# Kernel optimization log

Hardware: AMD Instinct MI355X
Metric: run time of the kernel (lower is better)

The kernel has to match this reference:

```python
import jax, jax.numpy as jnp
import numpy as np


def _conv3x3(x, w, b):
    # standard 3x3 conv, stride 1, padding 1 (NCHW / OIHW)
    y = jax.lax.conv_general_dilated(x, w, window_strides=(1, 1),
                                     padding=((1, 1), (1, 1)),
                                     dimension_numbers=('NCHW', 'OIHW', 'NCHW'))
    return y + b[None, :, None, None]


def _bilinear_gather(img, py, px):
    # img [B,C,H,W]; py/px [B,K,H,W] fractional sample coords; zero outside (torchvision semantics)
    B, C, H, W = img.shape
    K = py.shape[1]
    y0f = jnp.floor(py)
    x0f = jnp.floor(px)
    dy = py - y0f
    dx = px - x0f
    y0 = y0f.astype(jnp.int32)
    x0 = x0f.astype(jnp.int32)
    img_f = img.reshape(B, C, H * W)

    def corner(yy, xx, wgt):
        valid = (yy >= 0) & (yy < H) & (xx >= 0) & (xx < W)
        idx = (jnp.clip(yy, 0, H - 1) * W + jnp.clip(xx, 0, W - 1)).reshape(B, -1)
        g = jax.vmap(lambda im, ix: im[:, ix])(img_f, idx)  # [B, C, K*H*W]
        return g * (wgt * valid).reshape(B, 1, -1)

    out = (corner(y0, x0, (1 - dy) * (1 - dx)) + corner(y0, x0 + 1, (1 - dy) * dx)
           + corner(y0 + 1, x0, dy * (1 - dx)) + corner(y0 + 1, x0 + 1, dy * dx))
    return out.reshape(B, C, K, H, W)


def _deform_conv(x, offset, w, b):
    # torchvision DeformConv2d, kernel 3, stride 1, pad 1, no groups
    # offset [B, 2*K, H, W], channel pairs (2k, 2k+1) = (dy, dx) for tap k
    B, C, H, W = x.shape
    K = 9
    off = offset.reshape(B, K, 2, H, W)
    ki, kj = jnp.meshgrid(jnp.arange(3), jnp.arange(3), indexing='ij')
    ki = (ki.reshape(K) - 1).astype(x.dtype)
    kj = (kj.reshape(K) - 1).astype(x.dtype)
    py = jnp.arange(H, dtype=x.dtype)[None, None, :, None] + ki[None, :, None, None] + off[:, :, 0]
    px = jnp.arange(W, dtype=x.dtype)[None, None, None, :] + kj[None, :, None, None] + off[:, :, 1]
    patches = _bilinear_gather(x, py, px)  # [B, C, K, H, W]
    out = jnp.einsum('bckhw,ock->bohw', patches, w.reshape(w.shape[0], C, K))
    return out + b[None, :, None, None]


def _maxpool2(x):
    return jax.lax.reduce_window(x, -jnp.inf, jax.lax.max, (1, 1, 2, 2), (1, 1, 2, 2), 'VALID')


def _forward(x, w_off1, b_off1, w1, b1, w_off2, b_off2, w2, b2,
             w_off3, b_off3, w3, b3, w_fc, b_fc):
    off = _conv3x3(x, w_off1, b_off1)
    h = jax.nn.relu(_deform_conv(x, off, w1, b1))
    h = _maxpool2(h)                       # [B,16,48,48]
    off = _conv3x3(h, w_off2, b_off2)
    h = jax.nn.relu(_deform_conv(h, off, w2, b2))
    h = _maxpool2(h)                       # [B,32,24,24]
    off = _conv3x3(h, w_off3, b_off3)
    h = jax.nn.relu(_deform_conv(h, off, w3, b3))  # [B,64,24,24]
    B, C, H, W = h.shape
    # adaptive avg pool to (3,3): 24 -> 3 exact bins of 8
    h = h.reshape(B, C, 3, H // 3, 3, W // 3).mean(axis=(3, 5))
    h = h.reshape(B, -1)                   # [B, 576]
    return h @ w_fc.T + b_fc


def setup_inputs() -> dict:
    key = jax.random.key(0)
    ks = jax.random.split(key, 16)
    f32 = jnp.float32

    def rn(k, shape, scale):
        return jax.random.normal(k, shape, dtype=f32) * scale

    return {
        'x': rn(ks[0], (64, 1, 96, 96), 1.0),
        # offset convs: small weights so offsets start near zero (standard deform init)
        'w_off1': rn(ks[1], (18, 1, 3, 3), 0.01), 'b_off1': jnp.zeros((18,), f32),
        'w1': rn(ks[2], (16, 1, 3, 3), 1.0 / 3.0), 'b1': jnp.zeros((16,), f32),
        'w_off2': rn(ks[3], (18, 16, 3, 3), 0.01), 'b_off2': jnp.zeros((18,), f32),
        'w2': rn(ks[4], (32, 16, 3, 3), 1.0 / 12.0), 'b2': jnp.zeros((32,), f32),
        'w_off3': rn(ks[5], (18, 32, 3, 3), 0.01), 'b_off3': jnp.zeros((18,), f32),
        'w3': rn(ks[6], (64, 32, 3, 3), 1.0 / 17.0), 'b3': jnp.zeros((64,), f32),
        'w_fc': rn(ks[7], (10, 576), 1.0 / 24.0), 'b_fc': jnp.zeros((10,), f32),
    }


def reference(x, w_off1, b_off1, w1, b1, w_off2, b_off2, w2, b2,
              w_off3, b_off3, w3, b3, w_fc, b_fc):
    return _forward(x, w_off1, b_off1, w1, b1, w_off2, b_off2, w2, b2,
                    w_off3, b_off3, w3, b3, w_fc, b_fc)
```

## Files before the change

kernel.cpp:

```cpp
#include <hip/hip_runtime.h>
#include <math.h>


template <int CIN, int COUT>
__global__ void wtrans(const float* __restrict__ w, float* __restrict__ wT) {
  int t = blockIdx.x * 256 + threadIdx.x;
  if (t >= 9 * CIN * COUT) return;
  int k = t / (CIN * COUT);
  int r = t % (CIN * COUT);
  int c = r / COUT;
  int o = r % COUT;
  wT[t] = w[(o * CIN + c) * 9 + k];
}

__global__ void deform1_fused(const float* __restrict__ x,
                              const float* __restrict__ woff,
                              const float* __restrict__ boff,
                              const float* __restrict__ w1,
                              const float* __restrict__ b1,
                              float* __restrict__ out) {
  const int H = 96, W = 96, HW = H * W;
  __shared__ float wos[9 * 18];
  __shared__ __align__(16) float ws1[9 * 16];
  for (int t = threadIdx.x; t < 9 * 18; t += 256) { int k = t / 18, tc = t % 18; wos[t] = woff[tc * 9 + k]; }
  for (int t = threadIdx.x; t < 9 * 16; t += 256) { int k = t / 16, o = t % 16; ws1[t] = w1[o * 9 + k]; }
  __syncthreads();

  int gid = blockIdx.x * 256 + threadIdx.x;
  int p2 = gid % (HW / 2);
  int b  = gid / (HW / 2);
  int xi0 = (2 * p2) % W, yi = (2 * p2) / W;
  const float* xb = x + (size_t)b * HW;

  float v[3][4];
#pragma unroll
  for (int r = 0; r < 3; ++r) {
    int yy = yi + r - 1;
    float my = (yy >= 0 && yy < H) ? 1.f : 0.f;
    int cy = min(max(yy, 0), H - 1);
#pragma unroll
    for (int c = 0; c < 4; ++c) {
      int xx = xi0 + c - 1;
      float mx = (xx >= 0 && xx < W) ? 1.f : 0.f;
      int cx = min(max(xx, 0), W - 1);
      v[r][c] = xb[cy * W + cx] * (my * mx);
    }
  }

  float off0[18], off1[18];
#pragma unroll
  for (int tc = 0; tc < 18; ++tc) { float bb = boff[tc]; off0[tc] = bb; off1[tc] = bb; }
#pragma unroll
  for (int r = 0; r < 3; ++r)
#pragma unroll
    for (int c = 0; c < 3; ++c) {
      float t0 = v[r][c], t1 = v[r][c + 1];
      const float2* wv = (const float2*)&wos[(r * 3 + c) * 18];
#pragma unroll
      for (int tt = 0; tt < 9; ++tt) {
        float2 ww = wv[tt];
        off0[2 * tt]     = fmaf(ww.x, t0, off0[2 * tt]);
        off0[2 * tt + 1] = fmaf(ww.y, t0, off0[2 * tt + 1]);
        off1[2 * tt]     = fmaf(ww.x, t1, off1[2 * tt]);
        off1[2 * tt + 1] = fmaf(ww.y, t1, off1[2 * tt + 1]);
      }
    }

  float acc0[16], acc1[16];
#pragma unroll
  for (int o = 0; o < 16; ++o) { float bb = b1[o]; acc0[o] = bb; acc1[o] = bb; }

#pragma unroll
  for (int k = 0; k < 9; ++k) {
    int dky = k / 3 - 1, dkx = k % 3 - 1;
    float val0, val1;
    {
      float py = (float)(yi + dky) + off0[2 * k];
      float px = (float)(xi0 + dkx) + off0[2 * k + 1];
      float y0f = floorf(py), x0f = floorf(px);
      float fy = py - y0f, fx = px - x0f;
      int y0 = (int)y0f, x0 = (int)x0f, y1 = y0 + 1, x1 = x0 + 1;
      float vy0 = (y0 >= 0 && y0 < H) ? 1.f : 0.f;
      float vy1 = (y1 >= 0 && y1 < H) ? 1.f : 0.f;
      float vx0 = (x0 >= 0 && x0 < W) ? 1.f : 0.f;
      float vx1 = (x1 >= 0 && x1 < W) ? 1.f : 0.f;
      float w00 = (1.f - fy) * (1.f - fx) * vy0 * vx0;
      float w01 = (1.f - fy) * fx * vy0 * vx1;
      float w10 = fy * (1.f - fx) * vy1 * vx0;
      float w11 = fy * fx * vy1 * vx1;
      int cy0 = min(max(y0, 0), H - 1), cy1 = min(max(y1, 0), H - 1);
      int cx0 = min(max(x0, 0), W - 1), cx1 = min(max(x1, 0), W - 1);
      float a = xb[cy0 * W + cx0], bb = xb[cy0 * W + cx1];
      float c = xb[cy1 * W + cx0], d = xb[cy1 * W + cx1];
      val0 = w00 * a + w01 * bb + w10 * c + w11 * d;
    }
    {
      float py = (float)(yi + dky) + off1[2 * k];
      float px = (float)(xi0 + 1 + dkx) + off1[2 * k + 1];
      float y0f = floorf(py), x0f = floorf(px);
      float fy = py - y0f, fx = px - x0f;
      int y0 = (int)y0f, x0 = (int)x0f, y1 = y0 + 1, x1 = x0 + 1;
      float vy0 = (y0 >= 0 && y0 < H) ? 1.f : 0.f;
      float vy1 = (y1 >= 0 && y1 < H) ? 1.f : 0.f;
      float vx0 = (x0 >= 0 && x0 < W) ? 1.f : 0.f;
      float vx1 = (x1 >= 0 && x1 < W) ? 1.f : 0.f;
      float w00 = (1.f - fy) * (1.f - fx) * vy0 * vx0;
      float w01 = (1.f - fy) * fx * vy0 * vx1;
      float w10 = fy * (1.f - fx) * vy1 * vx0;
      float w11 = fy * fx * vy1 * vx1;
      int cy0 = min(max(y0, 0), H - 1), cy1 = min(max(y1, 0), H - 1);
      int cx0 = min(max(x0, 0), W - 1), cx1 = min(max(x1, 0), W - 1);
      float a = xb[cy0 * W + cx0], bb = xb[cy0 * W + cx1];
      float c = xb[cy1 * W + cx0], d = xb[cy1 * W + cx1];
      val1 = w00 * a + w01 * bb + w10 * c + w11 * d;
    }
    const float4* wv = (const float4*)&ws1[k * 16];
#pragma unroll
    for (int q = 0; q < 4; ++q) {
      float4 w4 = wv[q];
      acc0[4 * q + 0] = fmaf(w4.x, val0, acc0[4 * q + 0]);
      acc0[4 * q + 1] = fmaf(w4.y, val0, acc0[4 * q + 1]);
      acc0[4 * q + 2] = fmaf(w4.z, val0, acc0[4 * q + 2]);
      acc0[4 * q + 3] = fmaf(w4.w, val0, acc0[4 * q + 3]);
      acc1[4 * q + 0] = fmaf(w4.x, val1, acc1[4 * q + 0]);
      acc1[4 * q + 1] = fmaf(w4.y, val1, acc1[4 * q + 1]);
      acc1[4 * q + 2] = fmaf(w4.z, val1, acc1[4 * q + 2]);
      acc1[4 * q + 3] = fmaf(w4.w, val1, acc1[4 * q + 3]);
    }
  }

  float* op = out + (size_t)b * 16 * HW + (size_t)yi * W + xi0;
#pragma unroll
  for (int o = 0; o < 16; ++o) {
    float2 r = make_float2(fmaxf(acc0[o], 0.f), fmaxf(acc1[o], 0.f));
    *(float2*)(op + (size_t)o * HW) = r;
  }
}

template <int C, int HI>
__global__ void pool_nchw_to_nhwc(const float* __restrict__ in,
                                  float* __restrict__ out) {
  const int HO = HI / 2, C4 = C / 4;
  int gid = blockIdx.x * blockDim.x + threadIdx.x;
  if (gid >= 64 * HO * HO * C4) return;
  int c4 = gid % C4;
  int t = gid / C4;
  int x = t % HO; t /= HO;
  int y = t % HO;
  int b = t / HO;
  float4 r;
  float* rp = &r.x;
#pragma unroll
  for (int cc = 0; cc < 4; ++cc) {
    int c = c4 * 4 + cc;
    const float* p = in + ((size_t)(b * C + c) * HI + 2 * y) * HI + 2 * x;
    rp[cc] = fmaxf(fmaxf(p[0], p[1]), fmaxf(p[HI], p[HI + 1]));
  }
  *(float4*)(out + (((size_t)b * HO + y) * HO + x) * C + c4 * 4) = r;
}

template <int CIN, int COUT, int NSPLIT>
__global__ __launch_bounds__(256, 4)
void conv3x3_off(const float* __restrict__ in,
                 const float* __restrict__ w,
                 const float* __restrict__ bias,
                 float* __restrict__ out,
                 int B, int H, int W) {
  constexpr int OC = COUT / NSPLIT;
  __shared__ float ws[9 * CIN * OC];
  int obase = blockIdx.y * OC;
  for (int t = threadIdx.x; t < 9 * CIN * OC; t += 256) {
    int k = t / (CIN * OC); int r = t % (CIN * OC);
    int c = r / OC; int o = r % OC;
    ws[t] = w[((obase + o) * CIN + c) * 9 + k];
  }
  __syncthreads();

  int gid = blockIdx.x * 256 + threadIdx.x;
  if (gid >= B * H * W) return;
  int x = gid % W; int t0 = gid / W; int y = t0 % H; int b = t0 / H;
  int HW = H * W;
  const float* inb = in + (size_t)b * HW * CIN;

  float acc[OC];
#pragma unroll
  for (int o = 0; o < OC; ++o) acc[o] = bias[obase + o];

#pragma unroll
  for (int ky = 0; ky < 3; ++ky) {
    int yy = y + ky - 1;
    if (yy < 0 || yy >= H) continue;
#pragma unroll
    for (int kx = 0; kx < 3; ++kx) {
      int xx = x + kx - 1;
      if (xx < 0 || xx >= W) continue;
      const float4* p4 = (const float4*)(inb + ((size_t)yy * W + xx) * CIN);
      int k = ky * 3 + kx;
#pragma unroll
      for (int c4 = 0; c4 < CIN / 4; ++c4) {
        float4 p = p4[c4];
        const float* pv = &p.x;
#pragma unroll
        for (int cc = 0; cc < 4; ++cc) {
          const float* wrow = &ws[(k * CIN + 4 * c4 + cc) * OC];
#pragma unroll
          for (int o = 0; o < OC; ++o) acc[o] = fmaf(wrow[o], pv[cc], acc[o]);
        }
      }
    }
  }

  float* op = out + (size_t)gid * 20 + obase;
#pragma unroll
  for (int o = 0; o < OC; ++o) op[o] = acc[o];
}

template <int CIN, int COUT, int HW_, int PX>
__global__ void deform_patch(const float* __restrict__ in,
                             const float* __restrict__ off_in,
                             const float* __restrict__ wT,
                             const float* __restrict__ bias,
                             float* __restrict__ out) {
  constexpr int H = HW_, W = HW_, HW = H * W;
  constexpr int QT = CIN / 4;
  static_assert(PX * QT == 256, "block mapping");
  constexpr int PSTR = 9 * CIN + 4;
  constexpr int PP = PX / 2;
  constexpr int OG = 256 / PP;
  constexpr int OPG = COUT / OG;
  static_assert(OPG == 4, "phase2 mapping");

  __shared__ __align__(16) float offs[PX * 20];
  __shared__ __align__(16) float patch[PX * PSTR];
  __shared__ __align__(16) float wsk[CIN * COUT];

  const int pixbase = blockIdx.x * PX;
  const int b = pixbase / HW;
  const int p0_in_b = pixbase - b * HW;
  const float* inb = in + (size_t)b * HW * CIN;

  {
    const float4* src = (const float4*)(off_in + (size_t)pixbase * 20);
    for (int t = threadIdx.x; t < PX * 20 / 4; t += 256)
      ((float4*)offs)[t] = src[t];
  }
  __syncthreads();

  {
    int px = threadIdx.x % PX;
    int q  = threadIdx.x / PX;
    int pib = p0_in_b + px;
    int yi = pib / W, xi = pib % W;
#pragma unroll
    for (int k = 0; k < 9; ++k) {
      float py = (float)(yi + k / 3 - 1) + offs[px * 20 + 2 * k];
      float pxx = (float)(xi + k % 3 - 1) + offs[px * 20 + 2 * k + 1];
      float y0f = floorf(py), x0f = floorf(pxx);
      float fy = py - y0f, fx = pxx - x0f;
      int y0 = (int)y0f, x0 = (int)x0f, y1 = y0 + 1, x1 = x0 + 1;
      float vy0 = (y0 >= 0 && y0 < H) ? 1.f : 0.f;
      float vy1 = (y1 >= 0 && y1 < H) ? 1.f : 0.f;
      float vx0 = (x0 >= 0 && x0 < W) ? 1.f : 0.f;
      float vx1 = (x1 >= 0 && x1 < W) ? 1.f : 0.f;
      float w00 = (1.f - fy) * (1.f - fx) * vy0 * vx0;
      float w01 = (1.f - fy) * fx * vy0 * vx1;
      float w10 = fy * (1.f - fx) * vy1 * vx0;
      float w11 = fy * fx * vy1 * vx1;
      int cy0 = min(max(y0, 0), H - 1), cy1 = min(max(y1, 0), H - 1);
      int cx0 = min(max(x0, 0), W - 1), cx1 = min(max(x1, 0), W - 1);
      float4 A  = *(const float4*)(inb + ((size_t)cy0 * W + cx0) * CIN + 4 * q);
      float4 Bv = *(const float4*)(inb + ((size_t)cy0 * W + cx1) * CIN + 4 * q);
      float4 Cv = *(const float4*)(inb + ((size_t)cy1 * W + cx0) * CIN + 4 * q);
      float4 Dv = *(const float4*)(inb + ((size_t)cy1 * W + cx1) * CIN + 4 * q);
      float4 val;
      val.x = w00 * A.x + w01 * Bv.x + w10 * Cv.x + w11 * Dv.x;
      val.y = w00 * A.y + w01 * Bv.y + w10 * Cv.y + w11 * Dv.y;
      val.z = w00 * A.z + w01 * Bv.z + w10 * Cv.z + w11 * Dv.z;
      val.w = w00 * A.w + w01 * Bv.w + w10 * Cv.w + w11 * Dv.w;
      *(float4*)&patch[px * PSTR + k * CIN + 4 * q] = val;
    }
  }

  int pairIdx = threadIdx.x % PP;
  int og = threadIdx.x / PP;
  int obase = og * OPG;
  int px0 = pairIdx, px1 = pairIdx + PP;

  float acc0[OPG], acc1[OPG];
#pragma unroll
  for (int o = 0; o < OPG; ++o) { float bb = bias[obase + o]; acc0[o] = bb; acc1[o] = bb; }

  for (int k = 0; k < 9; ++k) {
    __syncthreads();
    {
      const float4* src = (const float4*)(wT + (size_t)k * CIN * COUT);
      for (int t = threadIdx.x; t < CIN * COUT / 4; t += 256)
        ((float4*)wsk)[t] = src[t];
    }
    __syncthreads();
#pragma unroll
    for (int c4 = 0; c4 < QT; ++c4) {
      float4 p0 = *(const float4*)&patch[px0 * PSTR + k * CIN + 4 * c4];
      float4 p1 = *(const float4*)&patch[px1 * PSTR + k * CIN + 4 * c4];
      const float* pv0 = &p0.x;
      const float* pv1 = &p1.x;
#pragma unroll
      for (int cc = 0; cc < 4; ++cc) {
        float4 wv = *(const float4*)&wsk[(4 * c4 + cc) * COUT + obase];
        acc0[0] = fmaf(wv.x, pv0[cc], acc0[0]);
        acc0[1] = fmaf(wv.y, pv0[cc], acc0[1]);
        acc0[2] = fmaf(wv.z, pv0[cc], acc0[2]);
        acc0[3] = fmaf(wv.w, pv0[cc], acc0[3]);
        acc1[0] = fmaf(wv.x, pv1[cc], acc1[0]);
        acc1[1] = fmaf(wv.y, pv1[cc], acc1[1]);
        acc1[2] = fmaf(wv.z, pv1[cc], acc1[2]);
        acc1[3] = fmaf(wv.w, pv1[cc], acc1[3]);
      }
    }
  }

  float* ob = out + ((size_t)b * COUT + obase) * HW + p0_in_b;
#pragma unroll
  for (int o = 0; o < OPG; ++o) {
    ob[(size_t)o * HW + px0] = fmaxf(acc0[o], 0.f);
    ob[(size_t)o * HW + px1] = fmaxf(acc1[o], 0.f);
  }
}

__global__ void poolfc_kernel(const float* __restrict__ h,
                              const float* __restrict__ wfc,
                              const float* __restrict__ bfc,
                              float* __restrict__ out) {
  __shared__ float feat[576];
  int b = blockIdx.x;
  int f = threadIdx.x;
  int c = f / 9, ij = f % 9, i = ij / 3, j = ij % 3;
  const float* p = h + ((size_t)(b * 64 + c) * 24 + i * 8) * 24 + j * 8;
  float s = 0.f;
#pragma unroll
  for (int r = 0; r < 8; ++r)
#pragma unroll
    for (int q = 0; q < 8; ++q)
      s += p[r * 24 + q];
  feat[f] = s * (1.f / 64.f);
  __syncthreads();
  if (f < 10) {
    float acc = bfc[f];
    const float* wp = wfc + f * 576;
    for (int t = 0; t < 576; ++t) acc = fmaf(wp[t], feat[t], acc);
    out[b * 10 + f] = acc;
  }
}

extern "C" void kernel_launch(void* const* d_in, const int* in_sizes, int n_in,
                              void* d_out, int out_size, void* d_ws, size_t ws_size,
                              hipStream_t stream) {
  const float* x      = (const float*)d_in[0];
  const float* w_off1 = (const float*)d_in[1];
  const float* b_off1 = (const float*)d_in[2];
  const float* w1     = (const float*)d_in[3];
  const float* b1     = (const float*)d_in[4];
  const float* w_off2 = (const float*)d_in[5];
  const float* b_off2 = (const float*)d_in[6];
  const float* w2     = (const float*)d_in[7];
  const float* b2     = (const float*)d_in[8];
  const float* w_off3 = (const float*)d_in[9];
  const float* b_off3 = (const float*)d_in[10];
  const float* w3     = (const float*)d_in[11];
  const float* b3     = (const float*)d_in[12];
  const float* w_fc   = (const float*)d_in[13];
  const float* b_fc   = (const float*)d_in[14];
  float* out = (float*)d_out;

  char* ws = (char*)d_ws;
  float* A   = (float*)(ws);
  float* Cp  = (float*)(ws + 18874368);
  float* Bp  = (float*)(ws + 37748736);
  float* wT2 = (float*)(ws + 47185920);
  float* wT3 = (float*)(ws + 47185920 + 9 * 16 * 32 * 4);

  const int thr = 256;

  wtrans<16, 32><<<(9 * 16 * 32 + 255) / 256, thr, 0, stream>>>(w2, wT2);
  wtrans<32, 64><<<(9 * 32 * 64 + 255) / 256, thr, 0, stream>>>(w3, wT3);

  deform1_fused<<<64 * 96 * 96 / 2 / thr, thr, 0, stream>>>(x, w_off1, b_off1, w1, b1, A);
  {
    int total = 64 * 48 * 48 * 4;
    pool_nchw_to_nhwc<16, 96><<<(total + thr - 1) / thr, thr, 0, stream>>>(A, Bp);
  }

  conv3x3_off<16, 18, 1><<<dim3(576, 1), thr, 0, stream>>>(Bp, w_off2, b_off2, Cp, 64, 48, 48);
  deform_patch<16, 32, 48, 64><<<64 * 48 * 48 / 64, thr, 0, stream>>>(Bp, Cp, wT2, b2, A);
  {
    int total = 64 * 24 * 24 * 8;
    pool_nchw_to_nhwc<32, 48><<<(total + thr - 1) / thr, thr, 0, stream>>>(A, Bp);
  }

  conv3x3_off<32, 18, 3><<<dim3(144, 3), thr, 0, stream>>>(Bp, w_off3, b_off3, Cp, 64, 24, 24);
  deform_patch<32, 64, 24, 32><<<64 * 24 * 24 / 32, thr, 0, stream>>>(Bp, Cp, wT3, b3, A);

  poolfc_kernel<<<64, 576, 0, stream>>>(A, w_fc, b_fc, out);
}
```

Measured before the change: 195.6 us.

## Read deform-conv weights via wave-uniform scalar loads instead of LDS staging

Result: slower. 213.5 us (+9.2%).

```diff
diff --git a/kernel.cpp b/kernel.cpp
--- a/kernel.cpp
+++ b/kernel.cpp
@@ -215,28 +215,25 @@
   for (int o = 0; o < OC; ++o) op[o] = acc[o];
 }
 
-template <int CIN, int COUT, int HW_, int PX>
-__global__ void deform_patch(const float* __restrict__ in,
-                             const float* __restrict__ off_in,
-                             const float* __restrict__ wT,
-                             const float* __restrict__ bias,
-                             float* __restrict__ out) {
+template <int CIN, int COUT, int HW_>
+__global__ void deform_sgpr(const float* __restrict__ in,
+                            const float* __restrict__ off_in,
+                            const float* __restrict__ wT,
+                            const float* __restrict__ bias,
+                            float* __restrict__ out) {
   constexpr int H = HW_, W = HW_, HW = H * W;
+  constexpr int PX = 64;
   constexpr int QT = CIN / 4;
-  static_assert(PX * QT == 256, "block mapping");
+  constexpr int QPT = QT / 4;
   constexpr int PSTR = 9 * CIN + 4;
-  constexpr int PP = PX / 2;
-  constexpr int OG = 256 / PP;
-  constexpr int OPG = COUT / OG;
-  static_assert(OPG == 4, "phase2 mapping");
+  constexpr int OPG = COUT / 4;
 
   __shared__ __align__(16) float offs[PX * 20];
   __shared__ __align__(16) float patch[PX * PSTR];
-  __shared__ __align__(16) float wsk[CIN * COUT];
 
   const int pixbase = blockIdx.x * PX;
   const int b = pixbase / HW;
-  const int p0_in_b = pixbase - b * HW;
+  const int p0 = pixbase - b * HW;
   const float* inb = in + (size_t)b * HW * CIN;
 
   {
@@ -247,13 +244,13 @@
   __syncthreads();
 
   {
-    int px = threadIdx.x % PX;
-    int q  = threadIdx.x / PX;
-    int pib = p0_in_b + px;
+    int px = threadIdx.x & 63;
+    int qp = threadIdx.x >> 6;
+    int pib = p0 + px;
     int yi = pib / W, xi = pib % W;
 #pragma unroll
     for (int k = 0; k < 9; ++k) {
-      float py = (float)(yi + k / 3 - 1) + offs[px * 20 + 2 * k];
+      float py  = (float)(yi + k / 3 - 1) + offs[px * 20 + 2 * k];
       float pxx = (float)(xi + k % 3 - 1) + offs[px * 20 + 2 * k + 1];
       float y0f = floorf(py), x0f = floorf(pxx);
       float fy = py - y0f, fx = pxx - x0f;
@@ -268,63 +265,55 @@
       float w11 = fy * fx * vy1 * vx1;
       int cy0 = min(max(y0, 0), H - 1), cy1 = min(max(y1, 0), H - 1);
       int cx0 = min(max(x0, 0), W - 1), cx1 = min(max(x1, 0), W - 1);
-      float4 A  = *(const float4*)(inb + ((size_t)cy0 * W + cx0) * CIN + 4 * q);
-      float4 Bv = *(const float4*)(inb + ((size_t)cy0 * W + cx1) * CIN + 4 * q);
-      float4 Cv = *(const float4*)(inb + ((size_t)cy1 * W + cx0) * CIN + 4 * q);
-      float4 Dv = *(const float4*)(inb + ((size_t)cy1 * W + cx1) * CIN + 4 * q);
-      float4 val;
-      val.x = w00 * A.x + w01 * Bv.x + w10 * Cv.x + w11 * Dv.x;
-      val.y = w00 * A.y + w01 * Bv.y + w10 * Cv.y + w11 * Dv.y;
-      val.z = w00 * A.z + w01 * Bv.z + w10 * Cv.z + w11 * Dv.z;
-      val.w = w00 * A.w + w01 * Bv.w + w10 * Cv.w + w11 * Dv.w;
-      *(float4*)&patch[px * PSTR + k * CIN + 4 * q] = val;
-    }
-  }
-
-  int pairIdx = threadIdx.x % PP;
-  int og = threadIdx.x / PP;
+      const float* r00 = inb + ((size_t)cy0 * W + cx0) * CIN;
+      const float* r01 = inb + ((size_t)cy0 * W + cx1) * CIN;
+      const float* r10 = inb + ((size_t)cy1 * W + cx0) * CIN;
+      const float* r11 = inb + ((size_t)cy1 * W + cx1) * CIN;
+#pragma unroll
+      for (int j = 0; j < QPT; ++j) {
+        int q = qp + j * 4;
+        float4 A  = *(const float4*)(r00 + 4 * q);
+        float4 Bv = *(const float4*)(r01 + 4 * q);
+        float4 Cv = *(const float4*)(r10 + 4 * q);
+        float4 Dv = *(const float4*)(r11 + 4 * q);
+        float4 val;
+        val.x = w00 * A.x + w01 * Bv.x + w10 * Cv.x + w11 * Dv.x;
+        val.y = w00 * A.y + w01 * Bv.y + w10 * Cv.y + w11 * Dv.y;
+        val.z = w00 * A.z + w01 * Bv.z + w10 * Cv.z + w11 * Dv.z;
+        val.w = w00 * A.w + w01 * Bv.w + w10 * Cv.w + w11 * Dv.w;
+        *(float4*)&patch[px * PSTR + k * CIN + 4 * q] = val;
+      }
+    }
+  }
+  __syncthreads();
+
+  int px = threadIdx.x & 63;
+  int og = __builtin_amdgcn_readfirstlane(threadIdx.x >> 6);
   int obase = og * OPG;
-  int px0 = pairIdx, px1 = pairIdx + PP;
-
-  float acc0[OPG], acc1[OPG];
-#pragma unroll
-  for (int o = 0; o < OPG; ++o) { float bb = bias[obase + o]; acc0[o] = bb; acc1[o] = bb; }
-
+
+  float acc[OPG];
+#pragma unroll
+  for (int o = 0; o < OPG; ++o) acc[o] = bias[obase + o];
+
+  const float* patp = &patch[px * PSTR];
   for (int k = 0; k < 9; ++k) {
-    __syncthreads();
-    {
-      const float4* src = (const float4*)(wT + (size_t)k * CIN * COUT);
-      for (int t = threadIdx.x; t < CIN * COUT / 4; t += 256)
-        ((float4*)wsk)[t] = src[t];
-    }
-    __syncthreads();
 #pragma unroll
     for (int c4 = 0; c4 < QT; ++c4) {
-      float4 p0 = *(const float4*)&patch[px0 * PSTR + k * CIN + 4 * c4];
-      float4 p1 = *(const float4*)&patch[px1 * PSTR + k * CIN + 4 * c4];
-      const float* pv0 = &p0.x;
-      const float* pv1 = &p1.x;
-#pragma unroll
-      for (int cc = 0; cc < 4; ++cc) {
-        float4 wv = *(const float4*)&wsk[(4 * c4 + cc) * COUT + obase];
-        acc0[0] = fmaf(wv.x, pv0[cc], acc0[0]);
-        acc0[1] = fmaf(wv.y, pv0[cc], acc0[1]);
-        acc0[2] = fmaf(wv.z, pv0[cc], acc0[2]);
-        acc0[3] = fmaf(wv.w, pv0[cc], acc0[3]);
-        acc1[0] = fmaf(wv.x, pv1[cc], acc1[0]);
-        acc1[1] = fmaf(wv.y, pv1[cc], acc1[1]);
-        acc1[2] = fmaf(wv.z, pv1[cc], acc1[2]);
-        acc1[3] = fmaf(wv.w, pv1[cc], acc1[3]);
-      }
-    }
-  }
-
-  float* ob = out + ((size_t)b * COUT + obase) * HW + p0_in_b;
-#pragma unroll
-  for (int o = 0; o < OPG; ++o) {
-    ob[(size_t)o * HW + px0] = fmaxf(acc0[o], 0.f);
-    ob[(size_t)o * HW + px1] = fmaxf(acc1[o], 0.f);
-  }
+      float4 p = *(const float4*)&patp[k * CIN + 4 * c4];
+      const float* pv = &p.x;
+      const float* wb = wT + ((size_t)(k * CIN + 4 * c4)) * COUT + obase;
+#pragma unroll
+      for (int cc = 0; cc < 4; ++cc)
+#pragma unroll
+        for (int o = 0; o < OPG; ++o)
+          acc[o] = fmaf(wb[cc * COUT + o], pv[cc], acc[o]);
+    }
+  }
+
+  float* ob = out + ((size_t)b * COUT + obase) * HW + p0 + px;
+#pragma unroll
+  for (int o = 0; o < OPG; ++o)
+    ob[(size_t)o * HW] = fmaxf(acc[o], 0.f);
 }
 
 __global__ void poolfc_kernel(const float* __restrict__ h,
@@ -391,14 +380,14 @@
   }
 
   conv3x3_off<16, 18, 1><<<dim3(576, 1), thr, 0, stream>>>(Bp, w_off2, b_off2, Cp, 64, 48, 48);
-  deform_patch<16, 32, 48, 64><<<64 * 48 * 48 / 64, thr, 0, stream>>>(Bp, Cp, wT2, b2, A);
+  deform_sgpr<16, 32, 48><<<64 * 48 * 48 / 64, thr, 0, stream>>>(Bp, Cp, wT2, b2, A);
   {
     int total = 64 * 24 * 24 * 8;
     pool_nchw_to_nhwc<32, 48><<<(total + thr - 1) / thr, thr, 0, stream>>>(A, Bp);
   }
 
   conv3x3_off<32, 18, 3><<<dim3(144, 3), thr, 0, stream>>>(Bp, w_off3, b_off3, Cp, 64, 24, 24);
-  deform_patch<32, 64, 24, 32><<<64 * 24 * 24 / 32, thr, 0, stream>>>(Bp, Cp, wT3, b3, A);
+  deform_sgpr<32, 64, 24><<<64 * 24 * 24 / 64, thr, 0, stream>>>(Bp, Cp, wT3, b3, A);
 
   poolfc_kernel<<<64, 576, 0, stream>>>(A, w_fc, b_fc, out);
 }
```
